# Optimization experiments

Hardware: AMD Instinct MI355X
Metric: run time of the kernel (lower is better)

## Reference

```python
import jax, jax.numpy as jnp
import numpy as np

IMAGE_DIM = 224


def setup_inputs() -> dict:
    key = jax.random.key(0)
    k1, k2, k3, k4, k5 = jax.random.split(key, 5)
    N, H, W = 64, IMAGE_DIM, IMAGE_DIM
    im1 = jax.random.normal(k1, (N, 3, H, W), dtype=jnp.float32)
    im2 = jax.random.normal(k2, (N, 3, H, W), dtype=jnp.float32)
    C = jax.random.normal(k3, (N, 2, H, W), dtype=jnp.float32)
    M1 = jax.random.uniform(k4, (N, 1, H, W), dtype=jnp.float32)
    M2 = jax.random.uniform(k5, (N, 1, H, W), dtype=jnp.float32)
    return {"im1": im1, "im2": im2, "C": C, "M1": M1, "M2": M2}


def _grid(dtype):
    # q = [repeat(arange(H), W), tile(arange(W), H)], shape [2, H*W]
    x = jnp.repeat(jnp.arange(IMAGE_DIM), IMAGE_DIM)
    y = jnp.tile(jnp.arange(IMAGE_DIM), IMAGE_DIM)
    return jnp.stack([x, y]).astype(dtype)  # [2, HW]


def _bilinear_sample(imflat, qi):
    # imflat: [N, 3, HW], qi: [N, 2, HW] float coords
    HW = imflat.shape[-1]
    px, py = qi[:, 0], qi[:, 1]  # [N, HW]
    fx, cx = jnp.floor(px), jnp.ceil(px)
    fy, cy = jnp.floor(py), jnp.ceil(py)

    def gather_pixel(nx, ny):
        # weight = prod over axes of (1 - |point - neighbor|)
        w = (1.0 - jnp.abs(px - nx)) * (1.0 - jnp.abs(py - ny))  # [N, HW]
        ind = (nx + IMAGE_DIM * ny).astype(jnp.int32)
        ind = jnp.clip(ind, 0, HW - 1)  # guard against out-of-range neighbors
        pix = jnp.take_along_axis(imflat, ind[:, None, :], axis=2)  # [N, 3, HW]
        return w[:, None, :] * pix

    return (gather_pixel(fx, fy) + gather_pixel(cx, fy)
            + gather_pixel(fx, cy) + gather_pixel(cy * 0 + cx, cy))


def reference(im1, im2, C, M1, M2):
    N, ch, H, W = im1.shape
    HW = H * W
    q = _grid(im1.dtype)[None]              # [1, 2, HW]
    Cflat = C.reshape(N, 2, HW)
    a = _bilinear_sample(im1.reshape(N, ch, HW), q + Cflat).reshape(N, ch, H, W) * M1
    b = _bilinear_sample(im2.reshape(N, ch, HW), q - Cflat).reshape(N, ch, H, W) * M2
    return a + b
```

## Files before the change

### kernel.cpp

```cpp
#include <hip/hip_runtime.h>

#define IMG 224
#define HW (IMG * IMG)
#define TILE 32
#define PAD 4
#define REG (TILE + 2 * PAD)
#define RST (REG + 1)
#define TSZ (REG * RST)
#define UT  (TILE * (TILE + 1))

__global__ __launch_bounds__(256, 4) void vm_kernel(
    const float* __restrict__ im1, const float* __restrict__ im2,
    const float* __restrict__ C, const float* __restrict__ M1,
    const float* __restrict__ M2, float* __restrict__ out)
{
    __shared__ float smem[6 * TSZ];

    const int n    = blockIdx.y;
    const int tile = blockIdx.x;
    const int x0   = (tile / 7) * TILE;
    const int y0   = (tile % 7) * TILE;
    const int t    = threadIdx.x;
    const int xlo  = x0 - PAD;
    const int ylo  = y0 - PAD;

    const float* Cn  = C  + (size_t)n * 2 * HW;
    const float* M1n = M1 + (size_t)n * HW;
    const float* M2n = M2 + (size_t)n * HW;

#pragma unroll
    for (int j = 0; j < 4; ++j) {
        int idx = t + 256 * j;
        int tx  = idx >> 5;
        int ty  = idx & 31;
        int p   = (x0 + tx) * IMG + (y0 + ty);
        smem[0 * UT + tx * 33 + ty] = Cn[p];
        smem[1 * UT + tx * 33 + ty] = Cn[HW + p];
        smem[2 * UT + tx * 33 + ty] = M1n[p];
        smem[3 * UT + tx * 33 + ty] = M2n[p];
    }
    __syncthreads();
    float c0[4], c1[4], m1v[4], m2v[4];
#pragma unroll
    for (int j = 0; j < 4; ++j) {
        int idx = t + 256 * j;
        int xl  = idx & 31;
        int yl  = idx >> 5;
        c0[j]  = smem[0 * UT + xl * 33 + yl];
        c1[j]  = smem[1 * UT + xl * 33 + yl];
        m1v[j] = smem[2 * UT + xl * 33 + yl];
        m2v[j] = smem[3 * UT + xl * 33 + yl];
    }
    __syncthreads();

    const float* i1n = im1 + (size_t)n * 3 * HW;
    const float* i2n = im2 + (size_t)n * 3 * HW;
    for (int e = t; e < REG * REG; e += 256) {
        int r  = e / REG;
        int c  = e - r * REG;
        int gi = (xlo + c) + IMG * (ylo + r);
        gi = min(max(gi, 0), HW - 1);
        int ls = r * RST + c;
#pragma unroll
        for (int ch = 0; ch < 3; ++ch) {
            smem[ch * TSZ + ls]       = i1n[ch * HW + gi];
            smem[(3 + ch) * TSZ + ls] = i2n[ch * HW + gi];
        }
    }
    __syncthreads();

    float res[12];
#pragma unroll
    for (int j = 0; j < 4; ++j) {
        int idx = t + 256 * j;
        int xl  = idx & 31;
        int yl  = idx >> 5;
        float xf = (float)(x0 + xl);
        float yf = (float)(y0 + yl);

        int   oA[4], oB[4];
        float wA[4], wB[4];
        int fa, fb;
        {
            float px = xf + c0[j], py = yf + c1[j];
            float fx = floorf(px), cx = ceilf(px);
            float fy = floorf(py), cy = ceilf(py);
            float wfx = 1.0f - (px - fx), wcx = 1.0f - (cx - px);
            float wfy = 1.0f - (py - fy), wcy = 1.0f - (cy - py);
            wA[0] = wfx * wfy; wA[1] = wcx * wfy;
            wA[2] = wfx * wcy; wA[3] = wcx * wcy;
            int gx0 = (int)fx, gy0 = (int)fy;
            int dx = (int)cx - gx0, dy = (int)cy - gy0;
            int q0 = gx0 - xlo, r0 = gy0 - ylo;
            int o  = r0 * RST + q0;
            oA[0] = o;            oA[1] = o + dx;
            oA[2] = o + dy * RST; oA[3] = o + dx + dy * RST;
            fa = __all((q0 >= 0) & (q0 + dx <= REG - 1) &
                       (r0 >= 0) & (r0 + dy <= REG - 1));
        }
        {
            float px = xf - c0[j], py = yf - c1[j];
            float fx = floorf(px), cx = ceilf(px);
            float fy = floorf(py), cy = ceilf(py);
            float wfx = 1.0f - (px - fx), wcx = 1.0f - (cx - px);
            float wfy = 1.0f - (py - fy), wcy = 1.0f - (cy - py);
            wB[0] = wfx * wfy; wB[1] = wcx * wfy;
            wB[2] = wfx * wcy; wB[3] = wcx * wcy;
            int gx0 = (int)fx, gy0 = (int)fy;
            int dx = (int)cx - gx0, dy = (int)cy - gy0;
            int q0 = gx0 - xlo, r0 = gy0 - ylo;
            int o  = r0 * RST + q0;
            oB[0] = o;            oB[1] = o + dx;
            oB[2] = o + dy * RST; oB[3] = o + dx + dy * RST;
            fb = __all((q0 >= 0) & (q0 + dx <= REG - 1) &
                       (r0 >= 0) & (r0 + dy <= REG - 1));
        }

        if (fa) {
#pragma unroll
            for (int ch = 0; ch < 3; ++ch) {
                const float* T = smem + ch * TSZ;
                res[j * 3 + ch] = m1v[j] *
                    (wA[0] * T[oA[0]] + wA[1] * T[oA[1]] +
                     wA[2] * T[oA[2]] + wA[3] * T[oA[3]]);
            }
        } else {
            float px = xf + c0[j], py = yf + c1[j];
            float fx = floorf(px), cx = ceilf(px);
            float fy = floorf(py), cy = ceilf(py);
            int i0 = min(max((int)fx + IMG * (int)fy, 0), HW - 1);
            int i1 = min(max((int)cx + IMG * (int)fy, 0), HW - 1);
            int i2 = min(max((int)fx + IMG * (int)cy, 0), HW - 1);
            int i3 = min(max((int)cx + IMG * (int)cy, 0), HW - 1);
#pragma unroll
            for (int ch = 0; ch < 3; ++ch) {
                const float* pa = i1n + ch * HW;
                res[j * 3 + ch] = m1v[j] *
                    (wA[0] * pa[i0] + wA[1] * pa[i1] +
                     wA[2] * pa[i2] + wA[3] * pa[i3]);
            }
        }
        if (fb) {
#pragma unroll
            for (int ch = 0; ch < 3; ++ch) {
                const float* T = smem + (3 + ch) * TSZ;
                res[j * 3 + ch] += m2v[j] *
                    (wB[0] * T[oB[0]] + wB[1] * T[oB[1]] +
                     wB[2] * T[oB[2]] + wB[3] * T[oB[3]]);
            }
        } else {
            float px = xf - c0[j], py = yf - c1[j];
            float fx = floorf(px), cx = ceilf(px);
            float fy = floorf(py), cy = ceilf(py);
            int i0 = min(max((int)fx + IMG * (int)fy, 0), HW - 1);
            int i1 = min(max((int)cx + IMG * (int)fy, 0), HW - 1);
            int i2 = min(max((int)fx + IMG * (int)cy, 0), HW - 1);
            int i3 = min(max((int)cx + IMG * (int)cy, 0), HW - 1);
#pragma unroll
            for (int ch = 0; ch < 3; ++ch) {
                const float* pb = i2n + ch * HW;
                res[j * 3 + ch] += m2v[j] *
                    (wB[0] * pb[i0] + wB[1] * pb[i1] +
                     wB[2] * pb[i2] + wB[3] * pb[i3]);
            }
        }
    }
    __syncthreads();

#pragma unroll
    for (int j = 0; j < 4; ++j) {
        int idx = t + 256 * j;
        int xl  = idx & 31;
        int yl  = idx >> 5;
#pragma unroll
        for (int ch = 0; ch < 3; ++ch)
            smem[ch * UT + xl * 33 + yl] = res[j * 3 + ch];
    }
    __syncthreads();
    float* on = out + (size_t)n * 3 * HW;
#pragma unroll
    for (int j = 0; j < 4; ++j) {
        int idx = t + 256 * j;
        int tx  = idx >> 5;
        int ty  = idx & 31;
        int p   = (x0 + tx) * IMG + (y0 + ty);
#pragma unroll
        for (int ch = 0; ch < 3; ++ch)
            on[ch * HW + p] = smem[ch * UT + tx * 33 + ty];
    }
}

extern "C" void kernel_launch(void* const* d_in, const int* in_sizes, int n_in,
                              void* d_out, int out_size, void* d_ws, size_t ws_size,
                              hipStream_t stream) {
    const float* im1 = (const float*)d_in[0];
    const float* im2 = (const float*)d_in[1];
    const float* C   = (const float*)d_in[2];
    const float* M1  = (const float*)d_in[3];
    const float* M2  = (const float*)d_in[4];
    float* out = (float*)d_out;
    dim3 grid(49, 64);
    vm_kernel<<<grid, 256, 0, stream>>>(im1, im2, C, M1, M2, out);
}
```

Before: 181.8 us.

## Drop shared-memory transposes and remap lanes to contiguous pixels

Result: faster. 173.0 us (-4.9%).

```diff
diff --git a/kernel.cpp b/kernel.cpp
--- a/kernel.cpp
+++ b/kernel.cpp
@@ -7,7 +7,6 @@
 #define REG (TILE + 2 * PAD)
 #define RST (REG + 1)
 #define TSZ (REG * RST)
-#define UT  (TILE * (TILE + 1))
 
 __global__ __launch_bounds__(256, 4) void vm_kernel(
     const float* __restrict__ im1, const float* __restrict__ im2,
@@ -24,59 +23,53 @@
     const int xlo  = x0 - PAD;
     const int ylo  = y0 - PAD;
 
+    const float* i1n = im1 + (size_t)n * 3 * HW;
+    const float* i2n = im2 + (size_t)n * 3 * HW;
     const float* Cn  = C  + (size_t)n * 2 * HW;
     const float* M1n = M1 + (size_t)n * HW;
     const float* M2n = M2 + (size_t)n * HW;
 
+#pragma unroll
+    for (int k = 0; k < 7; ++k) {
+        int e = t + 256 * k;
+        if (e < REG * REG) {
+            int r  = e / REG;
+            int c  = e - r * REG;
+            int gi = (xlo + c) + IMG * (ylo + r);
+            gi = min(max(gi, 0), HW - 1);
+            int ls = r * RST + c;
+#pragma unroll
+            for (int ch = 0; ch < 3; ++ch) {
+                smem[ch * TSZ + ls]       = i1n[ch * HW + gi];
+                smem[(3 + ch) * TSZ + ls] = i2n[ch * HW + gi];
+            }
+        }
+    }
+
+    float c0[4], c1[4], m1v[4], m2v[4];
 #pragma unroll
     for (int j = 0; j < 4; ++j) {
         int idx = t + 256 * j;
         int tx  = idx >> 5;
         int ty  = idx & 31;
         int p   = (x0 + tx) * IMG + (y0 + ty);
-        smem[0 * UT + tx * 33 + ty] = Cn[p];
-        smem[1 * UT + tx * 33 + ty] = Cn[HW + p];
-        smem[2 * UT + tx * 33 + ty] = M1n[p];
-        smem[3 * UT + tx * 33 + ty] = M2n[p];
+        c0[j]  = Cn[p];
+        c1[j]  = Cn[HW + p];
+        m1v[j] = M1n[p];
+        m2v[j] = M2n[p];
     }
+
     __syncthreads();
-    float c0[4], c1[4], m1v[4], m2v[4];
+
+    float* on = out + (size_t)n * 3 * HW;
 #pragma unroll
     for (int j = 0; j < 4; ++j) {
         int idx = t + 256 * j;
-        int xl  = idx & 31;
-        int yl  = idx >> 5;
-        c0[j]  = smem[0 * UT + xl * 33 + yl];
-        c1[j]  = smem[1 * UT + xl * 33 + yl];
-        m1v[j] = smem[2 * UT + xl * 33 + yl];
-        m2v[j] = smem[3 * UT + xl * 33 + yl];
-    }
-    __syncthreads();
-
-    const float* i1n = im1 + (size_t)n * 3 * HW;
-    const float* i2n = im2 + (size_t)n * 3 * HW;
-    for (int e = t; e < REG * REG; e += 256) {
-        int r  = e / REG;
-        int c  = e - r * REG;
-        int gi = (xlo + c) + IMG * (ylo + r);
-        gi = min(max(gi, 0), HW - 1);
-        int ls = r * RST + c;
-#pragma unroll
-        for (int ch = 0; ch < 3; ++ch) {
-            smem[ch * TSZ + ls]       = i1n[ch * HW + gi];
-            smem[(3 + ch) * TSZ + ls] = i2n[ch * HW + gi];
-        }
-    }
-    __syncthreads();
-
-    float res[12];
-#pragma unroll
-    for (int j = 0; j < 4; ++j) {
-        int idx = t + 256 * j;
-        int xl  = idx & 31;
-        int yl  = idx >> 5;
-        float xf = (float)(x0 + xl);
-        float yf = (float)(y0 + yl);
+        int tx  = idx >> 5;
+        int ty  = idx & 31;
+        int p   = (x0 + tx) * IMG + (y0 + ty);
+        float xf = (float)(x0 + tx);
+        float yf = (float)(y0 + ty);
 
         int   oA[4], oB[4];
         float wA[4], wB[4];
@@ -116,11 +109,12 @@
                        (r0 >= 0) & (r0 + dy <= REG - 1));
         }
 
+        float res[3];
         if (fa) {
 #pragma unroll
             for (int ch = 0; ch < 3; ++ch) {
                 const float* T = smem + ch * TSZ;
-                res[j * 3 + ch] = m1v[j] *
+                res[ch] = m1v[j] *
                     (wA[0] * T[oA[0]] + wA[1] * T[oA[1]] +
                      wA[2] * T[oA[2]] + wA[3] * T[oA[3]]);
             }
@@ -135,7 +129,7 @@
 #pragma unroll
             for (int ch = 0; ch < 3; ++ch) {
                 const float* pa = i1n + ch * HW;
-                res[j * 3 + ch] = m1v[j] *
+                res[ch] = m1v[j] *
                     (wA[0] * pa[i0] + wA[1] * pa[i1] +
                      wA[2] * pa[i2] + wA[3] * pa[i3]);
             }
@@ -144,7 +138,7 @@
 #pragma unroll
             for (int ch = 0; ch < 3; ++ch) {
                 const float* T = smem + (3 + ch) * TSZ;
-                res[j * 3 + ch] += m2v[j] *
+                res[ch] += m2v[j] *
                     (wB[0] * T[oB[0]] + wB[1] * T[oB[1]] +
                      wB[2] * T[oB[2]] + wB[3] * T[oB[3]]);
             }
@@ -159,34 +153,15 @@
 #pragma unroll
             for (int ch = 0; ch < 3; ++ch) {
                 const float* pb = i2n + ch * HW;
-                res[j * 3 + ch] += m2v[j] *
+                res[ch] += m2v[j] *
                     (wB[0] * pb[i0] + wB[1] * pb[i1] +
                      wB[2] * pb[i2] + wB[3] * pb[i3]);
             }
         }
-    }
-    __syncthreads();
 
 #pragma unroll
-    for (int j = 0; j < 4; ++j) {
-        int idx = t + 256 * j;
-        int xl  = idx & 31;
-        int yl  = idx >> 5;
-#pragma unroll
         for (int ch = 0; ch < 3; ++ch)
-            smem[ch * UT + xl * 33 + yl] = res[j * 3 + ch];
-    }
-    __syncthreads();
-    float* on = out + (size_t)n * 3 * HW;
-#pragma unroll
-    for (int j = 0; j < 4; ++j) {
-        int idx = t + 256 * j;
-        int tx  = idx >> 5;
-        int ty  = idx & 31;
-        int p   = (x0 + tx) * IMG + (y0 + ty);
-#pragma unroll
-        for (int ch = 0; ch < 3; ++ch)
-            on[ch * HW + p] = smem[ch * UT + tx * 33 + ty];
+            on[ch * HW + p] = res[ch];
     }
 }
 
```
